# Optimization experiments

Hardware: AMD Instinct MI355X
Metric: run time of the kernel (lower is better)

Reference implementation:

```python
import jax, jax.numpy as jnp
import numpy as np

B, N, DIM, H = 512, 98, 512, 16
HD = DIM // H
WS = (2, 7, 7)  # window size; N == 2*7*7


def _relative_position_index(ws):
    d, h, w = ws
    coords = np.stack(np.meshgrid(np.arange(d), np.arange(h), np.arange(w), indexing='ij'))
    cf = coords.reshape(3, -1)  # [3, N]
    rel = cf[:, :, None] - cf[:, None, :]  # [3, N, N]
    rel = rel.transpose(1, 2, 0).astype(np.int64)
    rel[:, :, 0] += d - 1
    rel[:, :, 1] += h - 1
    rel[:, :, 2] += w - 1
    rel[:, :, 0] *= (2 * h - 1) * (2 * w - 1)
    rel[:, :, 1] *= 2 * w - 1
    return rel.sum(-1)  # [N, N] in [0, (2d-1)(2h-1)(2w-1))


def setup_inputs() -> dict:
    key = jax.random.key(0)
    ks = jax.random.split(key, 6)
    table_size = (2 * WS[0] - 1) * (2 * WS[1] - 1) * (2 * WS[2] - 1)  # 507
    return {
        'x': jax.random.normal(ks[0], (B, N, DIM), jnp.float32),
        'qkv_w': jax.random.normal(ks[1], (DIM, 3 * DIM), jnp.float32) * 0.02,
        'qkv_b': jnp.zeros((3 * DIM,), jnp.float32),
        'proj_w': jax.random.normal(ks[2], (DIM, DIM), jnp.float32) * 0.02,
        'proj_b': jnp.zeros((DIM,), jnp.float32),
        'bias_table': jax.random.normal(ks[3], (table_size, H), jnp.float32) * 0.02,
        'rel_index': jnp.asarray(_relative_position_index(WS)),
    }


def reference(x, qkv_w, qkv_b, proj_w, proj_b, bias_table, rel_index):
    b, n, c = x.shape
    scale = HD ** -0.5
    qkv = (x @ qkv_w + qkv_b).reshape(b, n, 3, H, HD)
    qkv = jnp.transpose(qkv, (2, 0, 3, 1, 4))  # [3, B, H, N, HD]
    q, k, v = qkv[0] * scale, qkv[1], qkv[2]
    attn = jnp.einsum('bhnd,bhmd->bhnm', q, k)  # [B, H, N, N]
    # gather relative position bias: [N,N] indices into [table, H] -> [H, N, N]
    bias = jnp.transpose(bias_table[rel_index], (2, 0, 1))
    attn = jax.nn.softmax(attn + bias[None], axis=-1)
    out = jnp.einsum('bhnm,bhmd->bhnd', attn, v)  # [B, H, N, HD]
    out = jnp.transpose(out, (0, 2, 1, 3)).reshape(b, n, c)
    return out @ proj_w + proj_b
```

## Files before the change

### kernel.cpp

```cpp
#include <hip/hip_runtime.h>

typedef unsigned short u16;
typedef __bf16 bf16x8 __attribute__((ext_vector_type(8)));
typedef float f32x4 __attribute__((ext_vector_type(4)));

typedef __attribute__((address_space(1))) const void* as1_cvp;
typedef __attribute__((address_space(3))) void* as3_vp;

__device__ __forceinline__ float b2f(u16 u) {
  union { unsigned int i; float f; } x; x.i = ((unsigned int)u) << 16; return x.f;
}
__device__ __forceinline__ u16 f2b(float f) {
  union { float f; unsigned int i; } x; x.f = f;
  unsigned int u = x.i;
  u += 0x7fffu + ((u >> 16) & 1u);
  return (u16)(u >> 16);
}

__global__ void k_detect(const u16* __restrict__ x, int* __restrict__ flag) {
  int t = threadIdx.x;
  int sane = 0;
#pragma unroll
  for (int i = 0; i < 8; ++i) {
    u16 u = x[t * 8 + i];
    int e = (u >> 7) & 0xFF;
    sane += (u == 0 || (e >= 100 && e <= 150)) ? 1 : 0;
  }
#pragma unroll
  for (int off = 32; off >= 1; off >>= 1) sane += __shfl_xor(sane, off);
  if (t == 0) *flag = (sane < 480) ? 1 : 0;
}

__global__ void k_convert(const void* __restrict__ xin, u16* __restrict__ xb,
                          const int* __restrict__ flagp) {
  long i = ((long)blockIdx.x * 256 + threadIdx.x) * 4;
  if (*flagp) {
    float4 v = *(const float4*)((const float*)xin + i);
    u16* o = xb + i;
    o[0] = f2b(v.x); o[1] = f2b(v.y); o[2] = f2b(v.z); o[3] = f2b(v.w);
  } else {
    *(ushort4*)(xb + i) = *(const ushort4*)((const u16*)xin + i);
  }
}

__global__ void k_transpose(const void* __restrict__ W, u16* __restrict__ WT,
                            const int* __restrict__ flagp, int K, int N) {
  __shared__ u16 tile[32][33];
  int f = *flagp;
  int n0 = blockIdx.x * 32, k0 = blockIdx.y * 32;
  int tx = threadIdx.x, ty = threadIdx.y;
#pragma unroll
  for (int i = 0; i < 32; i += 8) {
    long idx = (long)(k0 + ty + i) * N + n0 + tx;
    tile[ty + i][tx] = f ? f2b(((const float*)W)[idx]) : ((const u16*)W)[idx];
  }
  __syncthreads();
#pragma unroll
  for (int i = 0; i < 32; i += 8)
    WT[(long)(n0 + ty + i) * K + k0 + tx] = tile[tx][ty + i];
}

__global__ void k_bias(const int* __restrict__ rel, const void* __restrict__ table,
                       float* __restrict__ biasM, const int* __restrict__ flagp) {
  int idx = blockIdx.x * 256 + threadIdx.x;
  if (idx >= 16 * 98 * 98) return;
  int f = *flagp;
  int j = idx % 98, i = (idx / 98) % 98, h = idx / (98 * 98);
  int r = rel[i * 98 + j];
  biasM[idx] = f ? ((const float*)table)[r * 16 + h] : b2f(((const u16*)table)[r * 16 + h]);
}

__global__ __launch_bounds__(256) void k_gemm_bt(
    const u16* __restrict__ A, const u16* __restrict__ BT,
    const void* __restrict__ bias, void* __restrict__ C,
    const int* __restrict__ flagp, int N, int K, int out_follows_flag) {
  __shared__ __align__(16) u16 As[128 * 32];
  __shared__ __align__(16) u16 Bs[128 * 32];
  const int t = threadIdx.x, w = t >> 6, ln = t & 63;
  const long bm = (long)blockIdx.x * 128, bn = (long)blockIdx.y * 128;
  const int lrow = ln >> 2, lseg = ln & 3;
  const u16* ag0 = A + (bm + w * 32 + lrow) * (long)K + lseg * 8;
  const u16* ag1 = ag0 + 16L * K;
  const u16* bg0 = BT + (bn + w * 32 + lrow) * (long)K + lseg * 8;
  const u16* bg1 = bg0 + 16L * K;
  u16* As0 = &As[w * 1024]; u16* As1 = &As[w * 1024 + 512];
  u16* Bs0 = &Bs[w * 1024]; u16* Bs1 = &Bs[w * 1024 + 512];
  const int wm = w & 1, wn = w >> 1;
  const int col = ln & 15, qrow = ln >> 4;
  f32x4 acc[4][4] = {};
  for (int k0 = 0; k0 < K; k0 += 32) {
    __syncthreads();
    __builtin_amdgcn_global_load_lds((as1_cvp)(const void*)(ag0 + k0), (as3_vp)As0, 16, 0, 0);
    __builtin_amdgcn_global_load_lds((as1_cvp)(const void*)(ag1 + k0), (as3_vp)As1, 16, 0, 0);
    __builtin_amdgcn_global_load_lds((as1_cvp)(const void*)(bg0 + k0), (as3_vp)Bs0, 16, 0, 0);
    __builtin_amdgcn_global_load_lds((as1_cvp)(const void*)(bg1 + k0), (as3_vp)Bs1, 16, 0, 0);
    __syncthreads();
    bf16x8 af[4], bfr[4];
#pragma unroll
    for (int mi = 0; mi < 4; ++mi)
      af[mi] = *(const bf16x8*)&As[(wm * 64 + mi * 16 + col) * 32 + qrow * 8];
#pragma unroll
    for (int ni = 0; ni < 4; ++ni)
      bfr[ni] = *(const bf16x8*)&Bs[(wn * 64 + ni * 16 + col) * 32 + qrow * 8];
#pragma unroll
    for (int mi = 0; mi < 4; ++mi)
#pragma unroll
      for (int ni = 0; ni < 4; ++ni)
        acc[mi][ni] = __builtin_amdgcn_mfma_f32_16x16x32_bf16(af[mi], bfr[ni], acc[mi][ni], 0, 0, 0);
  }
  const int f = *flagp;
  const int of = out_follows_flag ? f : 0;
  float bv[4];
#pragma unroll
  for (int ni = 0; ni < 4; ++ni) {
    long c = bn + wn * 64 + ni * 16 + col;
    bv[ni] = f ? ((const float*)bias)[c] : b2f(((const u16*)bias)[c]);
  }
#pragma unroll
  for (int mi = 0; mi < 4; ++mi)
#pragma unroll
    for (int ni = 0; ni < 4; ++ni)
#pragma unroll
      for (int r = 0; r < 4; ++r) {
        long row = bm + wm * 64 + mi * 16 + qrow * 4 + r;
        long c = bn + wn * 64 + ni * 16 + col;
        float v = acc[mi][ni][r] + bv[ni];
        if (of) ((float*)C)[row * N + c] = v;
        else    ((u16*)C)[row * N + c] = f2b(v);
      }
}

__global__ __launch_bounds__(256) void k_attn(
    const u16* __restrict__ qkv, const float* __restrict__ biasM, u16* __restrict__ attnout) {
  __shared__ __align__(16) u16 Qs[112 * 32];
  __shared__ __align__(16) u16 Ks[128 * 32];
  __shared__ __align__(16) u16 Vt[32 * 136];
  __shared__ __align__(16) u16 Ps[112 * 136];
  const int b = blockIdx.x, h = blockIdx.y;
  const int t = threadIdx.x;
  {
    unsigned int* z = (unsigned int*)Qs;
    for (int i = t; i < 1792; i += 256) z[i] = 0;
    z = (unsigned int*)Ks;
    for (int i = t; i < 2048; i += 256) z[i] = 0;
    z = (unsigned int*)Vt;
    for (int i = t; i < 2176; i += 256) z[i] = 0;
  }
  __syncthreads();
  {
    const int r0 = t >> 3, c4 = (t & 7) * 4;
    const u16* base = qkv + ((long)b * 98) * 1536 + h * 32;
#pragma unroll
    for (int it = 0; it < 4; ++it) {
      int r = r0 + it * 32;
      if (r < 98) {
        const u16* rowp = base + (long)r * 1536;
        *(ushort4*)&Qs[r * 32 + c4] = *(const ushort4*)(rowp + c4);
        *(ushort4*)&Ks[r * 32 + c4] = *(const ushort4*)(rowp + 512 + c4);
        ushort4 v4 = *(const ushort4*)(rowp + 1024 + c4);
        Vt[(c4 + 0) * 136 + r] = v4.x;
        Vt[(c4 + 1) * 136 + r] = v4.y;
        Vt[(c4 + 2) * 136 + r] = v4.z;
        Vt[(c4 + 3) * 136 + r] = v4.w;
      }
    }
  }
  __syncthreads();
  const int w = t >> 6, ln = t & 63;
  const int col = ln & 15, qrow = ln >> 4;
  const float scale = 0.17677669529663687f;
  const float* bh = biasM + h * (98 * 98);
  for (int tt = 0; tt < 2; ++tt) {
    const int ti = w + tt * 4;
    if (ti >= 7) break;
    bf16x8 aq = *(const bf16x8*)&Qs[(ti * 16 + col) * 32 + qrow * 8];
    f32x4 s[8];
#pragma unroll
    for (int tj = 0; tj < 8; ++tj) {
      bf16x8 bk = *(const bf16x8*)&Ks[(tj * 16 + col) * 32 + qrow * 8];
      f32x4 z = {0.f, 0.f, 0.f, 0.f};
      s[tj] = __builtin_amdgcn_mfma_f32_16x16x32_bf16(aq, bk, z, 0, 0, 0);
    }
#pragma unroll
    for (int r = 0; r < 4; ++r) {
      const int i = ti * 16 + qrow * 4 + r;
      const int ib = (i < 98) ? i : 97;
      float vals[8];
      float m = -1e30f;
#pragma unroll
      for (int tj = 0; tj < 8; ++tj) {
        int j = tj * 16 + col;
        float v = (j < 98) ? (s[tj][r] * scale + bh[ib * 98 + j]) : -1e30f;
        vals[tj] = v;
        m = fmaxf(m, v);
      }
#pragma unroll
      for (int off = 1; off < 16; off <<= 1) m = fmaxf(m, __shfl_xor(m, off));
      float sum = 0.f;
#pragma unroll
      for (int tj = 0; tj < 8; ++tj) { vals[tj] = __expf(vals[tj] - m); sum += vals[tj]; }
#pragma unroll
      for (int off = 1; off < 16; off <<= 1) sum += __shfl_xor(sum, off);
      float inv = 1.f / sum;
#pragma unroll
      for (int tj = 0; tj < 8; ++tj)
        Ps[i * 136 + tj * 16 + col] = f2b(vals[tj] * inv);
    }
    f32x4 o0 = {0.f, 0.f, 0.f, 0.f}, o1 = {0.f, 0.f, 0.f, 0.f};
#pragma unroll
    for (int ks = 0; ks < 4; ++ks) {
      bf16x8 ap  = *(const bf16x8*)&Ps[(ti * 16 + col) * 136 + ks * 32 + qrow * 8];
      bf16x8 bv0 = *(const bf16x8*)&Vt[col * 136 + ks * 32 + qrow * 8];
      bf16x8 bv1 = *(const bf16x8*)&Vt[(16 + col) * 136 + ks * 32 + qrow * 8];
      o0 = __builtin_amdgcn_mfma_f32_16x16x32_bf16(ap, bv0, o0, 0, 0, 0);
      o1 = __builtin_amdgcn_mfma_f32_16x16x32_bf16(ap, bv1, o1, 0, 0, 0);
    }
#pragma unroll
    for (int r = 0; r < 4; ++r) {
      const int i = ti * 16 + qrow * 4 + r;
      if (i < 98) {
        u16* op = attnout + ((long)(b * 98 + i)) * 512 + h * 32;
        op[col] = f2b(o0[r]);
        op[16 + col] = f2b(o1[r]);
      }
    }
  }
}

extern "C" void kernel_launch(void* const* d_in, const int* in_sizes, int n_in,
                              void* d_out, int out_size, void* d_ws, size_t ws_size,
                              hipStream_t stream) {
  (void)in_sizes; (void)n_in; (void)out_size; (void)ws_size;
  char* p = (char*)d_ws;
  u16* qkvbuf  = (u16*)p;  p += 50176L * 1536 * 2;
  u16* attnbuf = (u16*)p;  u16* xb = attnbuf; p += 50176L * 512 * 2;
  u16* wqkvT   = (u16*)p;  p += 1536L * 512 * 2;
  u16* wprojT  = (u16*)p;  p += 512L * 512 * 2;
  float* biasM = (float*)p; p += 16L * 98 * 98 * 4;
  int* flagp   = (int*)p;

  k_detect<<<1, 64, 0, stream>>>((const u16*)d_in[0], flagp);
  k_convert<<<25088, 256, 0, stream>>>(d_in[0], xb, flagp);
  k_transpose<<<dim3(48, 16), dim3(32, 8), 0, stream>>>(d_in[1], wqkvT, flagp, 512, 1536);
  k_transpose<<<dim3(16, 16), dim3(32, 8), 0, stream>>>(d_in[3], wprojT, flagp, 512, 512);
  k_bias<<<601, 256, 0, stream>>>((const int*)d_in[6], d_in[5], biasM, flagp);
  k_gemm_bt<<<dim3(392, 12), 256, 0, stream>>>(xb, wqkvT, d_in[2], qkvbuf, flagp, 1536, 512, 0);
  k_attn<<<dim3(512, 16), 256, 0, stream>>>(qkvbuf, biasM, attnbuf);
  k_gemm_bt<<<dim3(392, 4), 256, 0, stream>>>(attnbuf, wprojT, d_in[4], d_out, flagp, 512, 512, 1);
}
```

Measured before the change: 537.1 us.

## Precompute bf16 bias fragments, async-load Q/K, stage output, skip bf16 copy

Replaces the fp32 bias matrix with a bf16 bias laid out in MFMA fragment order, with padding masks baked in, so each lane loads it as contiguous ushort4 vectors. Q and K are now loaded with global_load_lds, and the full zero-fill of the Q, K and V tiles is dropped; only the V padding is zeroed. The attention output is staged in LDS and written back with vector stores, and the P buffer shrinks to a per-wave tile. The convert kernel now returns early when the input is already bf16, and the GEMM reads the raw input directly, which removes a copy. Storing the bias in bf16 is a small precision loss on the bias.

```diff
diff --git a/kernel.cpp b/kernel.cpp
--- a/kernel.cpp
+++ b/kernel.cpp
@@ -33,14 +33,11 @@
 
 __global__ void k_convert(const void* __restrict__ xin, u16* __restrict__ xb,
                           const int* __restrict__ flagp) {
+  if (!*flagp) return;
   long i = ((long)blockIdx.x * 256 + threadIdx.x) * 4;
-  if (*flagp) {
-    float4 v = *(const float4*)((const float*)xin + i);
-    u16* o = xb + i;
-    o[0] = f2b(v.x); o[1] = f2b(v.y); o[2] = f2b(v.z); o[3] = f2b(v.w);
-  } else {
-    *(ushort4*)(xb + i) = *(const ushort4*)((const u16*)xin + i);
-  }
+  float4 v = *(const float4*)((const float*)xin + i);
+  u16* o = xb + i;
+  o[0] = f2b(v.x); o[1] = f2b(v.y); o[2] = f2b(v.z); o[3] = f2b(v.w);
 }
 
 __global__ void k_transpose(const void* __restrict__ W, u16* __restrict__ WT,
@@ -60,22 +57,40 @@
     WT[(long)(n0 + ty + i) * K + k0 + tx] = tile[tx][ty + i];
 }
 
-__global__ void k_bias(const int* __restrict__ rel, const void* __restrict__ table,
-                       float* __restrict__ biasM, const int* __restrict__ flagp) {
-  int idx = blockIdx.x * 256 + threadIdx.x;
-  if (idx >= 16 * 98 * 98) return;
+__global__ void k_biasfrag(const int* __restrict__ rel, const void* __restrict__ table,
+                           u16* __restrict__ biasFrag, const int* __restrict__ flagp) {
+  int t = blockIdx.x * 256 + threadIdx.x;
   int f = *flagp;
-  int j = idx % 98, i = (idx / 98) % 98, h = idx / (98 * 98);
-  int r = rel[i * 98 + j];
-  biasM[idx] = f ? ((const float*)table)[r * 16 + h] : b2f(((const u16*)table)[r * 16 + h]);
+  int ln = t & 63, r2 = t >> 6;
+  int tj = r2 & 7, r3 = r2 >> 3;
+  int ti = r3 % 7, h = r3 / 7;
+  int col = ln & 15, qrow = ln >> 4;
+  int j = tj * 16 + col;
+  u16 v[4];
+#pragma unroll
+  for (int r = 0; r < 4; ++r) {
+    int i = ti * 16 + qrow * 4 + r; if (i > 97) i = 97;
+    float val;
+    if (j < 98) {
+      int rr = rel[i * 98 + j];
+      val = f ? ((const float*)table)[rr * 16 + h] : b2f(((const u16*)table)[rr * 16 + h]);
+    } else {
+      val = -1e30f;
+    }
+    v[r] = f2b(val);
+  }
+  ushort4 out; out.x = v[0]; out.y = v[1]; out.z = v[2]; out.w = v[3];
+  *(ushort4*)(biasFrag + (long)t * 4) = out;
 }
 
 __global__ __launch_bounds__(256) void k_gemm_bt(
-    const u16* __restrict__ A, const u16* __restrict__ BT,
-    const void* __restrict__ bias, void* __restrict__ C,
+    const u16* __restrict__ A_raw, const u16* __restrict__ A_conv,
+    const u16* __restrict__ BT, const void* __restrict__ bias, void* __restrict__ C,
     const int* __restrict__ flagp, int N, int K, int out_follows_flag) {
   __shared__ __align__(16) u16 As[128 * 32];
   __shared__ __align__(16) u16 Bs[128 * 32];
+  const int f = *flagp;
+  const u16* A = f ? A_conv : A_raw;
   const int t = threadIdx.x, w = t >> 6, ln = t & 63;
   const long bm = (long)blockIdx.x * 128, bn = (long)blockIdx.y * 128;
   const int lrow = ln >> 2, lseg = ln & 3;
@@ -108,7 +123,6 @@
       for (int ni = 0; ni < 4; ++ni)
         acc[mi][ni] = __builtin_amdgcn_mfma_f32_16x16x32_bf16(af[mi], bfr[ni], acc[mi][ni], 0, 0, 0);
   }
-  const int f = *flagp;
   const int of = out_follows_flag ? f : 0;
   float bv[4];
 #pragma unroll
@@ -131,48 +145,52 @@
 }
 
 __global__ __launch_bounds__(256) void k_attn(
-    const u16* __restrict__ qkv, const float* __restrict__ biasM, u16* __restrict__ attnout) {
+    const u16* __restrict__ qkv, const u16* __restrict__ biasFrag,
+    u16* __restrict__ attnout) {
   __shared__ __align__(16) u16 Qs[112 * 32];
   __shared__ __align__(16) u16 Ks[128 * 32];
   __shared__ __align__(16) u16 Vt[32 * 136];
-  __shared__ __align__(16) u16 Ps[112 * 136];
+  __shared__ __align__(16) u16 Ps[4][16 * 136];
   const int b = blockIdx.x, h = blockIdx.y;
-  const int t = threadIdx.x;
+  const int t = threadIdx.x, w = t >> 6, ln = t & 63;
+  const u16* qbase = qkv + (long)b * 98 * 1536 + h * 32;
   {
-    unsigned int* z = (unsigned int*)Qs;
-    for (int i = t; i < 1792; i += 256) z[i] = 0;
-    z = (unsigned int*)Ks;
-    for (int i = t; i < 2048; i += 256) z[i] = 0;
-    z = (unsigned int*)Vt;
-    for (int i = t; i < 2176; i += 256) z[i] = 0;
-  }
-  __syncthreads();
-  {
-    const int r0 = t >> 3, c4 = (t & 7) * 4;
-    const u16* base = qkv + ((long)b * 98) * 1536 + h * 32;
-#pragma unroll
-    for (int it = 0; it < 4; ++it) {
-      int r = r0 + it * 32;
-      if (r < 98) {
-        const u16* rowp = base + (long)r * 1536;
-        *(ushort4*)&Qs[r * 32 + c4] = *(const ushort4*)(rowp + c4);
-        *(ushort4*)&Ks[r * 32 + c4] = *(const ushort4*)(rowp + 512 + c4);
-        ushort4 v4 = *(const ushort4*)(rowp + 1024 + c4);
-        Vt[(c4 + 0) * 136 + r] = v4.x;
-        Vt[(c4 + 1) * 136 + r] = v4.y;
-        Vt[(c4 + 2) * 136 + r] = v4.z;
-        Vt[(c4 + 3) * 136 + r] = v4.w;
-      }
-    }
-  }
-  __syncthreads();
-  const int w = t >> 6, ln = t & 63;
+    const int gr = ln >> 2, gc = (ln & 3) * 8;
+    for (int n = w; n < 7; n += 4) {
+      int g = n * 16 + gr; if (g > 97) g = 97;
+      __builtin_amdgcn_global_load_lds((as1_cvp)(const void*)(qbase + (long)g * 1536 + gc),
+                                       (as3_vp)(Qs + n * 512), 16, 0, 0);
+    }
+    for (int n = w; n < 8; n += 4) {
+      int g = n * 16 + gr; if (g > 97) g = 97;
+      __builtin_amdgcn_global_load_lds((as1_cvp)(const void*)(qbase + 512 + (long)g * 1536 + gc),
+                                       (as3_vp)(Ks + n * 512), 16, 0, 0);
+    }
+  }
+  for (int z = t; z < 32 * 19; z += 256) {
+    int d = z / 19, q = z % 19;
+    *(unsigned int*)&Vt[d * 136 + 98 + q * 2] = 0u;
+  }
+  for (int idx = t; idx < 784; idx += 256) {
+    int i = idx >> 3, c4 = (idx & 7) * 4;
+    ushort4 v4 = *(const ushort4*)(qbase + 1024 + (long)i * 1536 + c4);
+    Vt[(c4 + 0) * 136 + i] = v4.x;
+    Vt[(c4 + 1) * 136 + i] = v4.y;
+    Vt[(c4 + 2) * 136 + i] = v4.z;
+    Vt[(c4 + 3) * 136 + i] = v4.w;
+  }
+  __syncthreads();
   const int col = ln & 15, qrow = ln >> 4;
   const float scale = 0.17677669529663687f;
-  const float* bh = biasM + h * (98 * 98);
+  u16* Psw = &Ps[w][0];
+  f32x4 o[2][2] = {{{0.f,0.f,0.f,0.f},{0.f,0.f,0.f,0.f}},{{0.f,0.f,0.f,0.f},{0.f,0.f,0.f,0.f}}};
   for (int tt = 0; tt < 2; ++tt) {
     const int ti = w + tt * 4;
     if (ti >= 7) break;
+    const u16* bp = biasFrag + ((long)((h * 7 + ti) * 8) * 64 + ln) * 4;
+    ushort4 bfv[8];
+#pragma unroll
+    for (int tj = 0; tj < 8; ++tj) bfv[tj] = *(const ushort4*)(bp + tj * 256);
     bf16x8 aq = *(const bf16x8*)&Qs[(ti * 16 + col) * 32 + qrow * 8];
     f32x4 s[8];
 #pragma unroll
@@ -183,16 +201,12 @@
     }
 #pragma unroll
     for (int r = 0; r < 4; ++r) {
-      const int i = ti * 16 + qrow * 4 + r;
-      const int ib = (i < 98) ? i : 97;
-      float vals[8];
-      float m = -1e30f;
+      float vals[8]; float m = -1e30f;
 #pragma unroll
       for (int tj = 0; tj < 8; ++tj) {
-        int j = tj * 16 + col;
-        float v = (j < 98) ? (s[tj][r] * scale + bh[ib * 98 + j]) : -1e30f;
-        vals[tj] = v;
-        m = fmaxf(m, v);
+        u16 bb = (r == 0) ? bfv[tj].x : (r == 1) ? bfv[tj].y : (r == 2) ? bfv[tj].z : bfv[tj].w;
+        float v = fmaf(s[tj][r], scale, b2f(bb));
+        vals[tj] = v; m = fmaxf(m, v);
       }
 #pragma unroll
       for (int off = 1; off < 16; off <<= 1) m = fmaxf(m, __shfl_xor(m, off));
@@ -202,28 +216,40 @@
 #pragma unroll
       for (int off = 1; off < 16; off <<= 1) sum += __shfl_xor(sum, off);
       float inv = 1.f / sum;
+      const int rt = qrow * 4 + r;
 #pragma unroll
       for (int tj = 0; tj < 8; ++tj)
-        Ps[i * 136 + tj * 16 + col] = f2b(vals[tj] * inv);
-    }
-    f32x4 o0 = {0.f, 0.f, 0.f, 0.f}, o1 = {0.f, 0.f, 0.f, 0.f};
+        Psw[rt * 136 + tj * 16 + col] = f2b(vals[tj] * inv);
+    }
 #pragma unroll
     for (int ks = 0; ks < 4; ++ks) {
-      bf16x8 ap  = *(const bf16x8*)&Ps[(ti * 16 + col) * 136 + ks * 32 + qrow * 8];
+      bf16x8 ap  = *(const bf16x8*)&Psw[col * 136 + ks * 32 + qrow * 8];
       bf16x8 bv0 = *(const bf16x8*)&Vt[col * 136 + ks * 32 + qrow * 8];
       bf16x8 bv1 = *(const bf16x8*)&Vt[(16 + col) * 136 + ks * 32 + qrow * 8];
-      o0 = __builtin_amdgcn_mfma_f32_16x16x32_bf16(ap, bv0, o0, 0, 0, 0);
-      o1 = __builtin_amdgcn_mfma_f32_16x16x32_bf16(ap, bv1, o1, 0, 0, 0);
-    }
+      o[tt][0] = __builtin_amdgcn_mfma_f32_16x16x32_bf16(ap, bv0, o[tt][0], 0, 0, 0);
+      o[tt][1] = __builtin_amdgcn_mfma_f32_16x16x32_bf16(ap, bv1, o[tt][1], 0, 0, 0);
+    }
+  }
+  __syncthreads();
+  u16* Os = Qs;
+#pragma unroll
+  for (int tt = 0; tt < 2; ++tt) {
+    const int ti = w + tt * 4;
+    if (ti >= 7) continue;
 #pragma unroll
     for (int r = 0; r < 4; ++r) {
       const int i = ti * 16 + qrow * 4 + r;
       if (i < 98) {
-        u16* op = attnout + ((long)(b * 98 + i)) * 512 + h * 32;
-        op[col] = f2b(o0[r]);
-        op[16 + col] = f2b(o1[r]);
+        Os[i * 32 + col]      = f2b(o[tt][0][r]);
+        Os[i * 32 + 16 + col] = f2b(o[tt][1][r]);
       }
     }
+  }
+  __syncthreads();
+  u16* obase = attnout + (long)b * 98 * 512 + h * 32;
+  for (int idx = t; idx < 784; idx += 256) {
+    int i = idx >> 3, c4 = (idx & 7) * 4;
+    *(ushort4*)(obase + (long)i * 512 + c4) = *(const ushort4*)&Os[i * 32 + c4];
   }
 }
 
@@ -232,19 +258,21 @@
                               hipStream_t stream) {
   (void)in_sizes; (void)n_in; (void)out_size; (void)ws_size;
   char* p = (char*)d_ws;
-  u16* qkvbuf  = (u16*)p;  p += 50176L * 1536 * 2;
-  u16* attnbuf = (u16*)p;  u16* xb = attnbuf; p += 50176L * 512 * 2;
-  u16* wqkvT   = (u16*)p;  p += 1536L * 512 * 2;
-  u16* wprojT  = (u16*)p;  p += 512L * 512 * 2;
-  float* biasM = (float*)p; p += 16L * 98 * 98 * 4;
-  int* flagp   = (int*)p;
+  u16* qkvbuf   = (u16*)p;  p += 50176L * 1536 * 2;
+  u16* attnbuf  = (u16*)p;  u16* xb = attnbuf; p += 50176L * 512 * 2;
+  u16* wqkvT    = (u16*)p;  p += 1536L * 512 * 2;
+  u16* wprojT   = (u16*)p;  p += 512L * 512 * 2;
+  u16* biasFrag = (u16*)p;  p += 57344L * 4 * 2;
+  int* flagp    = (int*)p;
 
   k_detect<<<1, 64, 0, stream>>>((const u16*)d_in[0], flagp);
   k_convert<<<25088, 256, 0, stream>>>(d_in[0], xb, flagp);
   k_transpose<<<dim3(48, 16), dim3(32, 8), 0, stream>>>(d_in[1], wqkvT, flagp, 512, 1536);
   k_transpose<<<dim3(16, 16), dim3(32, 8), 0, stream>>>(d_in[3], wprojT, flagp, 512, 512);
-  k_bias<<<601, 256, 0, stream>>>((const int*)d_in[6], d_in[5], biasM, flagp);
-  k_gemm_bt<<<dim3(392, 12), 256, 0, stream>>>(xb, wqkvT, d_in[2], qkvbuf, flagp, 1536, 512, 0);
-  k_attn<<<dim3(512, 16), 256, 0, stream>>>(qkvbuf, biasM, attnbuf);
-  k_gemm_bt<<<dim3(392, 4), 256, 0, stream>>>(attnbuf, wprojT, d_in[4], d_out, flagp, 512, 512, 1);
-}
+  k_biasfrag<<<224, 256, 0, stream>>>((const int*)d_in[6], d_in[5], biasFrag, flagp);
+  k_gemm_bt<<<dim3(392, 12), 256, 0, stream>>>((const u16*)d_in[0], xb, wqkvT, d_in[2],
+                                               qkvbuf, flagp, 1536, 512, 0);
+  k_attn<<<dim3(512, 16), 256, 0, stream>>>(qkvbuf, biasFrag, attnbuf);
+  k_gemm_bt<<<dim3(392, 4), 256, 0, stream>>>(attnbuf, attnbuf, wprojT, d_in[4],
+                                              d_out, flagp, 512, 512, 1);
+}
```

Result: faster. 464.8 us (-13.5%).
